# Performance work log

Measured on AMD Instinct MI355X. Metric: run time of the kernel, lower is better.

## Reference

```python
import jax, jax.numpy as jnp
import numpy as np

B, T, H = 64, 512, 32
D_CONTENT, D_DISTORT, D_MOTION = 4096, 512, 256
D_TOTAL = D_CONTENT + D_DISTORT + D_MOTION  # 4864
RED = 128
TIME_INTERVAL = 8  # conf.ADJACENT_INTERVAL assumed
TAUS = (8, 10, 12, 14, 16)
BETA = 0.5


def setup_inputs() -> dict:
    key = jax.random.key(0)
    ks = jax.random.split(key, 20)
    s = 0.02
    f32 = jnp.float32
    return {
        "motionFeat": jax.random.normal(ks[0], (B, T, D_MOTION), f32),
        "featContent": jax.random.normal(ks[1], (B, T, D_CONTENT), f32),
        "featDistort": jax.random.normal(ks[2], (B, T, D_DISTORT), f32),
        "inputLength": jax.random.randint(ks[3], (B,), 200, T + 1),
        "fc0_w": jax.random.normal(ks[4], (RED, D_TOTAL), f32) * s,
        "fc0_b": jnp.zeros((RED,), f32),
        "gru_wih_f": jax.random.normal(ks[5], (3 * H, RED), f32) * s,
        "gru_whh_f": jax.random.normal(ks[6], (3 * H, H), f32) * s,
        "gru_bih_f": jnp.zeros((3 * H,), f32),
        "gru_bhh_f": jnp.zeros((3 * H,), f32),
        "gru_wih_b": jax.random.normal(ks[7], (3 * H, RED), f32) * s,
        "gru_whh_b": jax.random.normal(ks[8], (3 * H, H), f32) * s,
        "gru_bih_b": jnp.zeros((3 * H,), f32),
        "gru_bhh_b": jnp.zeros((3 * H,), f32),
        "q_w": jax.random.normal(ks[9], (1, 2 * H), f32) * s,
        "q_b": jnp.zeros((1,), f32),
        "mem1_w": jax.random.normal(ks[10], (32, 2 * H), f32) * s,
        "mem1_b": jnp.zeros((32,), f32),
        "mem2_w": jax.random.normal(ks[11], (5, 32), f32) * s,
        "mem2_b": jnp.zeros((5,), f32),
    }


def _gru_dir(xg, Whh, bhh, mask):
    """xg: [B,T,3H] precomputed input gates; mask: [B,T] bool. Returns [B,T,H]."""
    def step(h, inp):
        xgt, mt = inp  # [B,3H], [B]
        hg = h @ Whh.T + bhh
        r = jax.nn.sigmoid(xgt[:, :H] + hg[:, :H])
        z = jax.nn.sigmoid(xgt[:, H:2 * H] + hg[:, H:2 * H])
        n = jnp.tanh(xgt[:, 2 * H:] + r * hg[:, 2 * H:])
        hn = (1.0 - z) * n + z * h
        h = jnp.where(mt[:, None], hn, h)
        return h, h
    h0 = jnp.zeros((xg.shape[0], H), xg.dtype)
    _, out = jax.lax.scan(step, h0, (jnp.swapaxes(xg, 0, 1), jnp.swapaxes(mask, 0, 1)))
    return jnp.swapaxes(out, 0, 1)


def _tp_score(qv, maskf, vlen, tau, beta=BETA):
    """Vectorized TP() + mean over valid frames. qv,maskf: [B,T]; vlen: [B]."""
    Bq, Tq = qv.shape
    # l: causal running min over last tau frames (front pad +inf in q-space)
    qpad = jnp.concatenate([jnp.full((Bq, tau - 1), jnp.inf, qv.dtype), qv], axis=1)
    l = jnp.min(jnp.stack([qpad[:, k:k + Tq] for k in range(tau)], 0), axis=0)
    # m/n: forward exp-weighted average over next tau frames; padding qp=1e4 -> exp(-1e4)=0
    w = jnp.exp(-qv) * maskf
    num = qv * w
    zpad = jnp.zeros((Bq, tau - 1), qv.dtype)
    npad = jnp.concatenate([num, zpad], axis=1)
    wpad = jnp.concatenate([w, zpad], axis=1)
    msum = sum(npad[:, k:k + Tq] for k in range(tau))
    nsum = sum(wpad[:, k:k + Tq] for k in range(tau))
    ratio = jnp.where(nsum > 0, msum / jnp.where(nsum > 0, nsum, 1.0), 0.0)
    pooled = beta * ratio + (1.0 - beta) * l
    return jnp.sum(pooled * maskf, axis=1) / vlen.astype(qv.dtype)


def reference(motionFeat, featContent, featDistort, inputLength,
              fc0_w, fc0_b, gru_wih_f, gru_whh_f, gru_bih_f, gru_bhh_f,
              gru_wih_b, gru_whh_b, gru_bih_b, gru_bhh_b,
              q_w, q_b, mem1_w, mem1_b, mem2_w, mem2_b):
    total = jnp.concatenate([featContent, featDistort, motionFeat], axis=-1)  # [B,T,4864]
    scores = total @ fc0_w.T + fc0_b  # ANN with n_ANNlayers=1 -> just fc0
    vlen = inputLength - 2 * (TIME_INTERVAL // 2) - 1  # [B]
    t = jnp.arange(T)
    mask = t[None, :] < vlen[:, None]  # [B,T] bool
    maskf = mask.astype(scores.dtype)
    # forward GRU
    xg_f = scores @ gru_wih_f.T + gru_bih_f
    out_f = _gru_dir(xg_f, gru_whh_f, gru_bhh_f, mask)
    # backward GRU: reverse each sequence within its valid length
    rev = jnp.where(mask, vlen[:, None] - 1 - t[None, :], t[None, :])  # [B,T]
    x_rev = jnp.take_along_axis(scores, rev[:, :, None], axis=1)
    xg_b = x_rev @ gru_wih_b.T + gru_bih_b
    out_b_rev = _gru_dir(xg_b, gru_whh_b, gru_bhh_b, mask)
    out_b = jnp.take_along_axis(out_b_rev, rev[:, :, None], axis=1)
    outputs = jnp.concatenate([out_f, out_b], axis=-1) * maskf[:, :, None]  # [B,T,64]
    lastHidForward = jnp.take_along_axis(out_f, (vlen - 1)[:, None, None], axis=1)[:, 0]  # [B,32]
    lastHidBackward = out_b[:, 0]  # [B,32]
    q = (outputs @ q_w.T + q_b)[..., 0]  # [B,T]
    hidcat = jnp.concatenate([lastHidForward, lastHidBackward], axis=-1)
    h1 = jax.nn.relu(hidcat @ mem1_w.T + mem1_b)
    param = jax.nn.softmax(h1 @ mem2_w.T + mem2_b, axis=-1)  # [B,5]
    scores5 = jnp.stack([_tp_score(q, maskf, vlen, tau) for tau in TAUS], axis=-1)  # [B,5]
    one_hot = jax.nn.one_hot(jnp.argmax(param, axis=1), 5, dtype=scores5.dtype)
    finalScores = jnp.sum(one_hot * scores5, axis=-1)  # [B]
    return finalScores
```

## Files before the change

kernel.cpp:

```cpp
#include <hip/hip_runtime.h>

typedef float  floatx4  __attribute__((ext_vector_type(4)));
typedef __bf16 bf16x8   __attribute__((ext_vector_type(8)));
typedef unsigned short ushort8v __attribute__((ext_vector_type(8)));

constexpr int NB = 64;
constexpr int NT = 512;
constexpr int DC = 4096, DD = 512, DM = 256, DTOT = 4864;
constexpr int RED = 128;
constexpr int MROWS = NB * NT;

__device__ __forceinline__ unsigned short f2bf(float f) {
  unsigned u = __float_as_uint(f);
  unsigned r = u + 0x7FFFu + ((u >> 16) & 1u);
  return (unsigned short)(r >> 16);
}

__device__ __forceinline__ ushort8v pack8(floatx4 a, floatx4 b) {
  ushort8v u;
  u[0] = f2bf(a[0]); u[1] = f2bf(a[1]); u[2] = f2bf(a[2]); u[3] = f2bf(a[3]);
  u[4] = f2bf(b[0]); u[5] = f2bf(b[1]); u[6] = f2bf(b[2]); u[7] = f2bf(b[3]);
  return u;
}

template<int MODE>
__global__ __launch_bounds__(256, 2) void gemm_bt(
    const float* __restrict__ A0, const float* __restrict__ A1, const float* __restrict__ A2,
    const float* __restrict__ W0, const float* __restrict__ W1,
    const float* __restrict__ bias0, const float* __restrict__ bias1,
    float* __restrict__ outp)
{
  constexpr int BN   = (MODE == 0) ? 128 : 192;
  constexpr int KTOT = (MODE == 0) ? DTOT : RED;
  constexpr int WNT  = (MODE == 0) ? 2 : 3;
  constexpr int BK   = 128;
  constexpr int ACH  = 64 * (BK / 8) / 256;
  constexpr int WCH  = BN * (BK / 8) / 256;

  __shared__ __align__(16) unsigned short As[64 * BK];
  __shared__ __align__(16) unsigned short Ws[BN * BK];

  const int tid  = threadIdx.x;
  const int lane = tid & 63;
  const int wave = tid >> 6;
  const int m0   = blockIdx.x * 64;

  floatx4 pa[2 * ACH], pw[2 * WCH];

  auto loadA = [&](int k0) {
    #pragma unroll
    for (int c = 0; c < ACH; ++c) {
      const int g   = c * 256 + tid;
      const int row = g >> 4;
      const int kk  = (g & 15) * 8;
      const int m   = m0 + row;
      const float* src;
      if (MODE == 0) {
        const int k = k0 + kk;
        if (k < DC)           src = A0 + (size_t)m * DC + k;
        else if (k < DC + DD) src = A1 + (size_t)m * DD + (k - DC);
        else                  src = A2 + (size_t)m * DM + (k - DC - DD);
      } else {
        src = A0 + (size_t)m * RED + (k0 + kk);
      }
      pa[2 * c]     = *(const floatx4*)(src);
      pa[2 * c + 1] = *(const floatx4*)(src + 4);
    }
  };
  auto loadW = [&](int k0) {
    #pragma unroll
    for (int c = 0; c < WCH; ++c) {
      const int g   = c * 256 + tid;
      const int row = g >> 4;
      const int kk  = (g & 15) * 8;
      const float* src;
      if (MODE == 0) {
        src = W0 + (size_t)row * DTOT + (k0 + kk);
      } else {
        src = (row < 96) ? (W0 + (size_t)row * RED + (k0 + kk))
                         : (W1 + (size_t)(row - 96) * RED + (k0 + kk));
      }
      pw[2 * c]     = *(const floatx4*)(src);
      pw[2 * c + 1] = *(const floatx4*)(src + 4);
    }
  };
  auto storeA = [&]() {
    #pragma unroll
    for (int c = 0; c < ACH; ++c) {
      const int g   = c * 256 + tid;
      const int row = g >> 4;
      const int kk  = (g & 15) * 8;
      *(ushort8v*)&As[row * BK + (kk ^ ((row & 15) * 8))] = pack8(pa[2 * c], pa[2 * c + 1]);
    }
  };
  auto storeW = [&]() {
    #pragma unroll
    for (int c = 0; c < WCH; ++c) {
      const int g   = c * 256 + tid;
      const int row = g >> 4;
      const int kk  = (g & 15) * 8;
      *(ushort8v*)&Ws[row * BK + (kk ^ ((row & 15) * 8))] = pack8(pw[2 * c], pw[2 * c + 1]);
    }
  };

  floatx4 acc[4][WNT];
  #pragma unroll
  for (int mt = 0; mt < 4; ++mt)
    #pragma unroll
    for (int nt = 0; nt < WNT; ++nt)
      acc[mt][nt] = (floatx4){0.f, 0.f, 0.f, 0.f};

  const int lrow = lane & 15;
  const int lko  = (lane >> 4) * 8;

  loadA(0); loadW(0);

  for (int k0 = 0; k0 < KTOT; k0 += BK) {
    storeA(); storeW();
    __syncthreads();
    if (k0 + BK < KTOT) { loadA(k0 + BK); loadW(k0 + BK); }
    #pragma unroll
    for (int kk = 0; kk < BK; kk += 32) {
      bf16x8 af[4];
      #pragma unroll
      for (int mt = 0; mt < 4; ++mt) {
        const int row = mt * 16 + lrow;
        af[mt] = __builtin_bit_cast(bf16x8,
            *(const ushort8v*)&As[row * BK + ((kk + lko) ^ ((row & 15) * 8))]);
      }
      #pragma unroll
      for (int nt = 0; nt < WNT; ++nt) {
        const int wrow = (wave * WNT + nt) * 16 + lrow;
        bf16x8 wf = __builtin_bit_cast(bf16x8,
            *(const ushort8v*)&Ws[wrow * BK + ((kk + lko) ^ ((wrow & 15) * 8))]);
        #pragma unroll
        for (int mt = 0; mt < 4; ++mt)
          acc[mt][nt] = __builtin_amdgcn_mfma_f32_16x16x32_bf16(af[mt], wf, acc[mt][nt], 0, 0, 0);
      }
    }
    __syncthreads();
  }

  #pragma unroll
  for (int nt = 0; nt < WNT; ++nt) {
    const int n = (wave * WNT + nt) * 16 + lrow;
    const float bv = (MODE == 0) ? bias0[n]
                                 : ((n < 96) ? bias0[n] : bias1[n - 96]);
    #pragma unroll
    for (int mt = 0; mt < 4; ++mt) {
      const int mr = m0 + mt * 16 + (lane >> 4) * 4;
      #pragma unroll
      for (int r = 0; r < 4; ++r)
        outp[(size_t)(mr + r) * BN + n] = acc[mt][nt][r] + bv;
    }
  }
}

__global__ __launch_bounds__(64) void gru_kernel(
    const float* __restrict__ xg,
    const float* __restrict__ whh_f, const float* __restrict__ whh_b,
    const float* __restrict__ bhh_f, const float* __restrict__ bhh_b,
    const int* __restrict__ inputLength,
    float* __restrict__ outfb)
{
  const int b   = blockIdx.x >> 1;
  const int dir = blockIdx.x & 1;
  const int l   = threadIdx.x;
  const int vlen = inputLength[b] - 9;

  const float* whh = dir ? whh_b : whh_f;
  const float* bhh = dir ? bhh_b : bhh_f;

  __shared__ __align__(16) float hsh[32];

  float wr[32], wz[32], wn[32];
  float br = 0.f, bz = 0.f, bn = 0.f;
  if (l < 32) {
    br = bhh[l]; bz = bhh[32 + l]; bn = bhh[64 + l];
    #pragma unroll
    for (int j = 0; j < 32; ++j) {
      wr[j] = whh[l * 32 + j];
      wz[j] = whh[(32 + l) * 32 + j];
      wn[j] = whh[(64 + l) * 32 + j];
    }
    hsh[l] = 0.f;
  } else {
    #pragma unroll
    for (int j = 0; j < 32; ++j) { wr[j] = 0.f; wz[j] = 0.f; wn[j] = 0.f; }
  }

  for (int t = 0; t < vlen; ++t) {
    const int time = dir ? (vlen - 1 - t) : t;
    const float* xr = xg + ((size_t)(b * NT + time)) * 192 + dir * 96;

    float xv_r = 0.f, xv_z = 0.f, xv_n = 0.f, hl = 0.f;
    if (l < 32) {
      xv_r = xr[l]; xv_z = xr[32 + l]; xv_n = xr[64 + l];
      hl = hsh[l];
    }

    float h[32];
    #pragma unroll
    for (int i = 0; i < 8; ++i)
      *(floatx4*)&h[4 * i] = *(const floatx4*)&hsh[4 * i];

    float pr0 = br, pr1 = 0.f, pz0 = bz, pz1 = 0.f, pn0 = bn, pn1 = 0.f;
    #pragma unroll
    for (int j = 0; j < 16; ++j) {
      pr0 += wr[j] * h[j];       pr1 += wr[16 + j] * h[16 + j];
      pz0 += wz[j] * h[j];       pz1 += wz[16 + j] * h[16 + j];
      pn0 += wn[j] * h[j];       pn1 += wn[16 + j] * h[16 + j];
    }

    if (l < 32) {
      const float r  = 1.f / (1.f + __expf(-(xv_r + pr0 + pr1)));
      const float z  = 1.f / (1.f + __expf(-(xv_z + pz0 + pz1)));
      const float n  = tanhf(xv_n + r * (pn0 + pn1));
      const float hn = (1.f - z) * n + z * hl;
      hsh[l] = hn;
      outfb[((size_t)(b * NT + time)) * 64 + dir * 32 + l] = hn;
    }
  }
}

__global__ __launch_bounds__(256) void q_kernel(
    const float* __restrict__ outfb, const float* __restrict__ q_w,
    const float* __restrict__ q_b, const int* __restrict__ inputLength,
    float* __restrict__ qv)
{
  const int m = blockIdx.x * 256 + threadIdx.x;
  const int b = m >> 9, t = m & 511;
  const int vlen = inputLength[b] - 9;
  float acc = 0.f;
  if (t < vlen) {
    acc = q_b[0];
    const float* row = outfb + (size_t)m * 64;
    #pragma unroll
    for (int j = 0; j < 64; ++j) acc += row[j] * q_w[j];
  }
  qv[m] = acc;
}

__global__ __launch_bounds__(64) void final_kernel(
    const float* __restrict__ qv, const float* __restrict__ outfb,
    const int* __restrict__ inputLength,
    const float* __restrict__ m1w, const float* __restrict__ m1b,
    const float* __restrict__ m2w, const float* __restrict__ m2b,
    float* __restrict__ fin)
{
  const int b = blockIdx.x;
  const int tid = threadIdx.x;
  const int vlen = inputLength[b] - 9;

  __shared__ float qs[NT];
  __shared__ float es[NT];
  __shared__ float h1[32];
  __shared__ int tau_s;

  for (int t = tid; t < vlen; t += 64) {
    const float v = qv[b * NT + t];
    qs[t] = v;
    es[t] = expf(-v);
  }

  if (tid < 32) {
    const float* hf = outfb + (size_t)(b * NT + (vlen - 1)) * 64;
    const float* hb = outfb + (size_t)(b * NT) * 64 + 32;
    float a = m1b[tid];
    #pragma unroll
    for (int j = 0; j < 32; ++j) a += m1w[tid * 64 + j] * hf[j];
    #pragma unroll
    for (int j = 0; j < 32; ++j) a += m1w[tid * 64 + 32 + j] * hb[j];
    h1[tid] = fmaxf(a, 0.f);
  }
  __syncthreads();
  if (tid == 0) {
    float best = -3.4e38f; int bi = 0;
    for (int i = 0; i < 5; ++i) {
      float lg = m2b[i];
      for (int j = 0; j < 32; ++j) lg += m2w[i * 32 + j] * h1[j];
      if (lg > best) { best = lg; bi = i; }
    }
    tau_s = 8 + 2 * bi;
  }
  __syncthreads();
  const int tau = tau_s;

  float partial = 0.f;
  for (int t = tid; t < vlen; t += 64) {
    float msum = 0.f, nsum = 0.f;
    const int kmax = (tau < vlen - t) ? tau : (vlen - t);
    for (int k = 0; k < kmax; ++k) { msum += qs[t + k] * es[t + k]; nsum += es[t + k]; }
    const float ratio = (nsum > 0.f) ? (msum / nsum) : 0.f;
    float l = 3.4e38f;
    const int kb = (tau <= t + 1) ? tau : (t + 1);
    for (int k = 0; k < kb; ++k) l = fminf(l, qs[t - k]);
    partial += 0.5f * ratio + 0.5f * l;
  }
  #pragma unroll
  for (int off = 32; off > 0; off >>= 1)
    partial += __shfl_down(partial, off);
  if (tid == 0) fin[b] = partial / (float)vlen;
}

extern "C" void kernel_launch(void* const* d_in, const int* in_sizes, int n_in,
                              void* d_out, int out_size, void* d_ws, size_t ws_size,
                              hipStream_t stream)
{
  const float* motion  = (const float*)d_in[0];
  const float* content = (const float*)d_in[1];
  const float* distort = (const float*)d_in[2];
  const int*   ilen    = (const int*)d_in[3];
  const float* fc0_w = (const float*)d_in[4];
  const float* fc0_b = (const float*)d_in[5];
  const float* wih_f = (const float*)d_in[6];
  const float* whh_f = (const float*)d_in[7];
  const float* bih_f = (const float*)d_in[8];
  const float* bhh_f = (const float*)d_in[9];
  const float* wih_b = (const float*)d_in[10];
  const float* whh_b = (const float*)d_in[11];
  const float* bih_b = (const float*)d_in[12];
  const float* bhh_b = (const float*)d_in[13];
  const float* q_w  = (const float*)d_in[14];
  const float* q_b  = (const float*)d_in[15];
  const float* m1w  = (const float*)d_in[16];
  const float* m1b  = (const float*)d_in[17];
  const float* m2w  = (const float*)d_in[18];
  const float* m2b  = (const float*)d_in[19];

  char* ws = (char*)d_ws;
  float* scores = (float*)(ws);
  float* xg     = (float*)(ws + (size_t)MROWS * RED * 4);
  float* outfb  = (float*)(ws + (size_t)MROWS * (RED + 192) * 4);
  float* qv     = (float*)(ws + (size_t)MROWS * (RED + 192 + 64) * 4);

  gemm_bt<0><<<dim3(MROWS / 64), dim3(256), 0, stream>>>(
      content, distort, motion, fc0_w, nullptr, fc0_b, nullptr, scores);
  gemm_bt<1><<<dim3(MROWS / 64), dim3(256), 0, stream>>>(
      scores, nullptr, nullptr, wih_f, wih_b, bih_f, bih_b, xg);
  gru_kernel<<<dim3(NB * 2), dim3(64), 0, stream>>>(
      xg, whh_f, whh_b, bhh_f, bhh_b, ilen, outfb);
  q_kernel<<<dim3(MROWS / 256), dim3(256), 0, stream>>>(outfb, q_w, q_b, ilen, qv);
  final_kernel<<<dim3(NB), dim3(64), 0, stream>>>(
      qv, outfb, ilen, m1w, m1b, m2w, m2b, (float*)d_out);
}
```

Measured before the change: 1.110 ms.

## Fuse q projection into GRU, split matvec across wave halves, prefetch gates

The GRU kernel now splits each hidden-row dot product across both 32-lane halves of the wave, combines the halves with a cross-half shuffle, and prefetches input gates two steps ahead. The q projection is computed inside the recurrence with a wave reduction. Per-direction partial q values and the final hidden states are written out, which removes the separate q_kernel and the full outfb buffer. tanh is replaced by an exp-based formula. The recurrence is serial, so the intent is shorter per-step latency, at the cost of extra shuffle reductions on every step.

```diff
diff --git a/kernel.cpp b/kernel.cpp
--- a/kernel.cpp
+++ b/kernel.cpp
@@ -1,6 +1,7 @@
 #include <hip/hip_runtime.h>
 
 typedef float  floatx4  __attribute__((ext_vector_type(4)));
+typedef float  floatx2  __attribute__((ext_vector_type(2)));
 typedef __bf16 bf16x8   __attribute__((ext_vector_type(8)));
 typedef unsigned short ushort8v __attribute__((ext_vector_type(8)));
 
@@ -160,12 +161,16 @@
     const float* __restrict__ xg,
     const float* __restrict__ whh_f, const float* __restrict__ whh_b,
     const float* __restrict__ bhh_f, const float* __restrict__ bhh_b,
+    const float* __restrict__ q_w,
     const int* __restrict__ inputLength,
-    float* __restrict__ outfb)
+    float* __restrict__ qpart,
+    float* __restrict__ hid)
 {
-  const int b   = blockIdx.x >> 1;
-  const int dir = blockIdx.x & 1;
-  const int l   = threadIdx.x;
+  const int b    = blockIdx.x >> 1;
+  const int dir  = blockIdx.x & 1;
+  const int l    = threadIdx.x;
+  const int half = l >> 5;
+  const int row  = l & 31;
   const int vlen = inputLength[b] - 9;
 
   const float* whh = dir ? whh_b : whh_f;
@@ -173,76 +178,95 @@
 
   __shared__ __align__(16) float hsh[32];
 
-  float wr[32], wz[32], wn[32];
-  float br = 0.f, bz = 0.f, bn = 0.f;
+  floatx2 wr[8], wz[8], wn[8];
+  #pragma unroll
+  for (int j = 0; j < 8; ++j) {
+    const int c = 16 * half + 2 * j;
+    wr[j] = *(const floatx2*)&whh[(size_t)row        * 32 + c];
+    wz[j] = *(const floatx2*)&whh[(size_t)(32 + row) * 32 + c];
+    wn[j] = *(const floatx2*)&whh[(size_t)(64 + row) * 32 + c];
+  }
+  const float br = bhh[row], bz = bhh[32 + row], bn = bhh[64 + row];
+  const float qw = q_w[dir * 32 + row];
+
+  if (l < 32) hsh[l] = 0.f;
+  __syncthreads();
+
+  auto xaddr = [&](int tt) {
+    const int time = dir ? (vlen - 1 - tt) : tt;
+    return xg + (size_t)(b * NT + time) * 192 + dir * 96;
+  };
+  float c_r = 0.f, c_z = 0.f, c_n = 0.f, n_r = 0.f, n_z = 0.f, n_n = 0.f;
   if (l < 32) {
-    br = bhh[l]; bz = bhh[32 + l]; bn = bhh[64 + l];
-    #pragma unroll
-    for (int j = 0; j < 32; ++j) {
-      wr[j] = whh[l * 32 + j];
-      wz[j] = whh[(32 + l) * 32 + j];
-      wn[j] = whh[(64 + l) * 32 + j];
-    }
-    hsh[l] = 0.f;
-  } else {
-    #pragma unroll
-    for (int j = 0; j < 32; ++j) { wr[j] = 0.f; wz[j] = 0.f; wn[j] = 0.f; }
-  }
-
+    const float* x0 = xaddr(0);
+    c_r = x0[l]; c_z = x0[32 + l]; c_n = x0[64 + l];
+    if (vlen > 1) {
+      const float* x1 = xaddr(1);
+      n_r = x1[l]; n_z = x1[32 + l]; n_n = x1[64 + l];
+    }
+  }
+
+  float* qout = qpart + (size_t)dir * (NB * NT) + (size_t)b * NT;
+
+  float hl = 0.f;
   for (int t = 0; t < vlen; ++t) {
     const int time = dir ? (vlen - 1 - t) : t;
-    const float* xr = xg + ((size_t)(b * NT + time)) * 192 + dir * 96;
-
-    float xv_r = 0.f, xv_z = 0.f, xv_n = 0.f, hl = 0.f;
+
+    float f_r = 0.f, f_z = 0.f, f_n = 0.f;
+    if (t + 2 < vlen && l < 32) {
+      const float* x2 = xaddr(t + 2);
+      f_r = x2[l]; f_z = x2[32 + l]; f_n = x2[64 + l];
+    }
+
+    float h[16];
+    #pragma unroll
+    for (int i = 0; i < 4; ++i)
+      *(floatx4*)&h[4 * i] = *(const floatx4*)&hsh[16 * half + 4 * i];
+    const floatx2* h2 = (const floatx2*)h;
+
+    floatx2 ar = {0.f, 0.f}, az = {0.f, 0.f}, an = {0.f, 0.f};
+    floatx2 ar1 = {0.f, 0.f}, az1 = {0.f, 0.f}, an1 = {0.f, 0.f};
+    #pragma unroll
+    for (int j = 0; j < 4; ++j) {
+      ar  += wr[j]     * h2[j];     ar1 += wr[4 + j] * h2[4 + j];
+      az  += wz[j]     * h2[j];     az1 += wz[4 + j] * h2[4 + j];
+      an  += wn[j]     * h2[j];     an1 += wn[4 + j] * h2[4 + j];
+    }
+    float pr = ar[0] + ar[1] + ar1[0] + ar1[1];
+    float pz = az[0] + az[1] + az1[0] + az1[1];
+    float pn = an[0] + an[1] + an1[0] + an1[1];
+    pr += __shfl_xor(pr, 32);
+    pz += __shfl_xor(pz, 32);
+    pn += __shfl_xor(pn, 32);
+
+    float hn = hl;
     if (l < 32) {
-      xv_r = xr[l]; xv_z = xr[32 + l]; xv_n = xr[64 + l];
-      hl = hsh[l];
-    }
-
-    float h[32];
-    #pragma unroll
-    for (int i = 0; i < 8; ++i)
-      *(floatx4*)&h[4 * i] = *(const floatx4*)&hsh[4 * i];
-
-    float pr0 = br, pr1 = 0.f, pz0 = bz, pz1 = 0.f, pn0 = bn, pn1 = 0.f;
-    #pragma unroll
-    for (int j = 0; j < 16; ++j) {
-      pr0 += wr[j] * h[j];       pr1 += wr[16 + j] * h[16 + j];
-      pz0 += wz[j] * h[j];       pz1 += wz[16 + j] * h[16 + j];
-      pn0 += wn[j] * h[j];       pn1 += wn[16 + j] * h[16 + j];
-    }
-
-    if (l < 32) {
-      const float r  = 1.f / (1.f + __expf(-(xv_r + pr0 + pr1)));
-      const float z  = 1.f / (1.f + __expf(-(xv_z + pz0 + pz1)));
-      const float n  = tanhf(xv_n + r * (pn0 + pn1));
-      const float hn = (1.f - z) * n + z * hl;
+      const float r = 1.f / (1.f + __expf(-(c_r + pr + br)));
+      const float z = 1.f / (1.f + __expf(-(c_z + pz + bz)));
+      const float e = __expf(-2.f * (c_n + r * (pn + bn)));
+      const float n = 2.f / (1.f + e) - 1.f;
+      hn = (1.f - z) * n + z * hl;
+      hl = hn;
       hsh[l] = hn;
-      outfb[((size_t)(b * NT + time)) * 64 + dir * 32 + l] = hn;
-    }
-  }
-}
-
-__global__ __launch_bounds__(256) void q_kernel(
-    const float* __restrict__ outfb, const float* __restrict__ q_w,
-    const float* __restrict__ q_b, const int* __restrict__ inputLength,
-    float* __restrict__ qv)
-{
-  const int m = blockIdx.x * 256 + threadIdx.x;
-  const int b = m >> 9, t = m & 511;
-  const int vlen = inputLength[b] - 9;
-  float acc = 0.f;
-  if (t < vlen) {
-    acc = q_b[0];
-    const float* row = outfb + (size_t)m * 64;
-    #pragma unroll
-    for (int j = 0; j < 64; ++j) acc += row[j] * q_w[j];
-  }
-  qv[m] = acc;
+    }
+
+    float qp = (l < 32) ? hn * qw : 0.f;
+    #pragma unroll
+    for (int off = 16; off > 0; off >>= 1)
+      qp += __shfl_xor(qp, off);
+    if (l == 0) qout[time] = qp;
+
+    if (t == vlen - 1 && l < 32) hid[b * 64 + dir * 32 + l] = hn;
+
+    c_r = n_r; c_z = n_z; c_n = n_n;
+    n_r = f_r; n_z = f_z; n_n = f_n;
+  }
 }
 
 __global__ __launch_bounds__(64) void final_kernel(
-    const float* __restrict__ qv, const float* __restrict__ outfb,
+    const float* __restrict__ qf, const float* __restrict__ qb,
+    const float* __restrict__ hid,
+    const float* __restrict__ q_b,
     const int* __restrict__ inputLength,
     const float* __restrict__ m1w, const float* __restrict__ m1b,
     const float* __restrict__ m2w, const float* __restrict__ m2b,
@@ -251,6 +275,7 @@
   const int b = blockIdx.x;
   const int tid = threadIdx.x;
   const int vlen = inputLength[b] - 9;
+  const float qb0 = q_b[0];
 
   __shared__ float qs[NT];
   __shared__ float es[NT];
@@ -258,14 +283,14 @@
   __shared__ int tau_s;
 
   for (int t = tid; t < vlen; t += 64) {
-    const float v = qv[b * NT + t];
+    const float v = qf[b * NT + t] + qb[b * NT + t] + qb0;
     qs[t] = v;
     es[t] = expf(-v);
   }
 
   if (tid < 32) {
-    const float* hf = outfb + (size_t)(b * NT + (vlen - 1)) * 64;
-    const float* hb = outfb + (size_t)(b * NT) * 64 + 32;
+    const float* hf = hid + b * 64;
+    const float* hb = hid + b * 64 + 32;
     float a = m1b[tid];
     #pragma unroll
     for (int j = 0; j < 32; ++j) a += m1w[tid * 64 + j] * hf[j];
@@ -331,16 +356,16 @@
   char* ws = (char*)d_ws;
   float* scores = (float*)(ws);
   float* xg     = (float*)(ws + (size_t)MROWS * RED * 4);
-  float* outfb  = (float*)(ws + (size_t)MROWS * (RED + 192) * 4);
-  float* qv     = (float*)(ws + (size_t)MROWS * (RED + 192 + 64) * 4);
+  float* qpart  = (float*)(ws + (size_t)MROWS * (RED + 192) * 4);
+  float* hid    = (float*)(ws + (size_t)MROWS * (RED + 192) * 4
+                              + (size_t)2 * MROWS * 4);
 
   gemm_bt<0><<<dim3(MROWS / 64), dim3(256), 0, stream>>>(
       content, distort, motion, fc0_w, nullptr, fc0_b, nullptr, scores);
   gemm_bt<1><<<dim3(MROWS / 64), dim3(256), 0, stream>>>(
       scores, nullptr, nullptr, wih_f, wih_b, bih_f, bih_b, xg);
   gru_kernel<<<dim3(NB * 2), dim3(64), 0, stream>>>(
-      xg, whh_f, whh_b, bhh_f, bhh_b, ilen, outfb);
-  q_kernel<<<dim3(MROWS / 256), dim3(256), 0, stream>>>(outfb, q_w, q_b, ilen, qv);
+      xg, whh_f, whh_b, bhh_f, bhh_b, q_w, ilen, qpart, hid);
   final_kernel<<<dim3(NB), dim3(64), 0, stream>>>(
-      qv, outfb, ilen, m1w, m1b, m2w, m2b, (float*)d_out);
-}
+      qpart, qpart + (size_t)NB * NT, hid, q_b, ilen, m1w, m1b, m2w, m2b, (float*)d_out);
+}
```

Result: no change. 1.116 ms (+0.6%).
